# Kernel tuning notes

Measured on AMD Instinct MI355X. Metric: run time of the kernel, lower is better.

Reference implementation:

```python
import jax, jax.numpy as jnp
import numpy as np

N_QUBITS = 10
N_LAYERS = 3
DIM = 2 ** N_QUBITS
B = 2048
T1, T2, GATE_TIME = 0.05, 0.07, 1e-07
P_GATE_1Q, P_GATE_2Q, P_READOUT = 0.001, 0.01, 0.02
P_AMP = 1.0 - np.exp(-GATE_TIME / T1)
P_PHASE = 1.0 - np.exp(-GATE_TIME / T2)

_I = np.eye(2, dtype=np.complex64)
_X = np.array([[0, 1], [1, 0]], np.complex64)
_Y = np.array([[0, -1j], [1j, 0]], np.complex64)
_Z = np.array([[1, 0], [0, -1]], np.complex64)

def _depol(p):
    return [np.sqrt(1 - p) * _I, np.sqrt(p / 3) * _X, np.sqrt(p / 3) * _Y, np.sqrt(p / 3) * _Z]

def _ampdamp(g):
    return [np.array([[1, 0], [0, np.sqrt(1 - g)]], np.complex64), np.array([[0, np.sqrt(g)], [0, 0]], np.complex64)]

def _phasedamp(g):
    return [np.array([[1, 0], [0, np.sqrt(1 - g)]], np.complex64), np.array([[0, 0], [0, np.sqrt(g)]], np.complex64)]

def _bitflip(p):
    return [np.sqrt(1 - p) * _I, np.sqrt(p) * _X]

DEPOL1 = [jnp.asarray(k) for k in _depol(P_GATE_1Q)]
DEPOL2 = [jnp.asarray(k) for k in _depol(P_GATE_2Q)]
AMP = [jnp.asarray(k) for k in _ampdamp(P_AMP)]
PHASE = [jnp.asarray(k) for k in _phasedamp(P_PHASE)]
BITFLIP = [jnp.asarray(k) for k in _bitflip(P_READOUT)]
CNOT = jnp.asarray(np.array([[1, 0, 0, 0], [0, 1, 0, 0], [0, 0, 0, 1], [0, 0, 1, 0]], np.complex64).reshape(2, 2, 2, 2))

def pauli_strings(n):
    out = []
    for q in range(n):
        for ch in 'XZ':
            out.append('I' * q + ch + 'I' * (n - q - 1))
    return out

def pauli_tensor(strings):
    mats = {'I': np.eye(2), 'X': np.array([[0., 1.], [1., 0.]]), 'Z': np.array([[1., 0.], [0., -1.]])}
    Ps = []
    for s in strings:
        P = np.array([[1.0]])
        for ch in s:
            P = np.kron(P, mats[ch])
        Ps.append(P)
    return np.stack(Ps).astype(np.float32)

def _apply1(rho, K, q, n):
    # rho' = K rho K^dagger on wire q; rho has shape (2,)*2n (ket axes 0..n-1, bra axes n..2n-1)
    rho = jnp.moveaxis(jnp.tensordot(K, rho, axes=[[1], [q]]), 0, q)
    rho = jnp.moveaxis(jnp.tensordot(jnp.conj(K), rho, axes=[[1], [n + q]]), 0, n + q)
    return rho

def _apply2(rho, U, q1, q2, n):
    rho = jnp.moveaxis(jnp.tensordot(U, rho, axes=[[2, 3], [q1, q2]]), [0, 1], [q1, q2])
    rho = jnp.moveaxis(jnp.tensordot(jnp.conj(U), rho, axes=[[2, 3], [n + q1, n + q2]]), [0, 1], [n + q1, n + q2])
    return rho

def _chan1(rho, Ks, q, n):
    out = _apply1(rho, Ks[0], q, n)
    for K in Ks[1:]:
        out = out + _apply1(rho, K, q, n)
    return out

def _rot(phi, theta, omega):
    # qml.Rot = RZ(omega) @ RY(theta) @ RZ(phi)
    c = jnp.cos(theta / 2).astype(jnp.complex64)
    s = jnp.sin(theta / 2).astype(jnp.complex64)
    ep = jnp.exp(-0.5j * (phi + omega))
    em = jnp.exp(0.5j * (phi - omega))
    return jnp.stack([jnp.stack([ep * c, -em * s]), jnp.stack([jnp.conj(em) * s, jnp.conj(ep) * c])])

def _simulate(weights):
    nl, nq, _ = weights.shape
    rho = jnp.zeros((2,) * (2 * nq), jnp.complex64).at[(0,) * (2 * nq)].set(1.0)
    for l in range(nl):
        for q in range(nq):
            rho = _apply1(rho, _rot(weights[l, q, 0], weights[l, q, 1], weights[l, q, 2]), q, nq)
            rho = _chan1(rho, DEPOL1, q, nq)
            rho = _chan1(rho, AMP, q, nq)
            rho = _chan1(rho, PHASE, q, nq)
        for q in range(nq):
            t = (q + 1) % nq
            rho = _apply2(rho, CNOT, q, t, nq)
            for wq in (q, t):
                rho = _chan1(rho, DEPOL2, wq, nq)
            for wq in (q, t):
                rho = _chan1(rho, AMP, wq, nq)
            for wq in (q, t):
                rho = _chan1(rho, PHASE, wq, nq)
    for q in range(nq):
        rho = _chan1(rho, BITFLIP, q, nq)
    return rho.reshape(2 ** nq, 2 ** nq)

def setup_inputs() -> dict:
    key = jax.random.key(0)
    k1, k2, k3 = jax.random.split(key, 3)
    x = jax.random.normal(k1, (B, DIM), jnp.float32)
    circuit_weights = jax.random.uniform(k2, (N_LAYERS, N_QUBITS, 3), jnp.float32)
    w = jax.random.normal(k3, (2 * N_QUBITS,), jnp.float32) * 0.01
    b = jnp.zeros((DIM,), jnp.float32)
    P_tensor = jnp.asarray(pauli_tensor(pauli_strings(N_QUBITS)))  # [K, dim, dim]
    return {"x": x, "b": b, "w": w, "circuit_weights": circuit_weights, "P_tensor": P_tensor}

def reference(x, b, w, circuit_weights, P_tensor):
    x_t = x + b  # [B, dim]
    feats = jnp.einsum('bm,kmn,bn->bk', x_t, P_tensor, x_t)  # [B, K]
    rho = _simulate(circuit_weights)  # [dim, dim] complex
    exps = jnp.real(jnp.einsum('kmn,nm->k', P_tensor.astype(jnp.complex64), rho))  # tr(P_k rho)
    logits = jnp.sum(feats * (w * exps), axis=1)
    return jax.nn.sigmoid(logits)
```

## Files before the change

### kernel.cpp

```cpp
#include <hip/hip_runtime.h>
#include <hip/hip_bf16.h>
#include <math.h>

struct cf { float x, y; };
__device__ __forceinline__ cf cfmul(cf a, cf b){ return {a.x*b.x - a.y*b.y, a.x*b.y + a.y*b.x}; }
__device__ __forceinline__ cf cfconj(cf a){ return {a.x, -a.y}; }
__device__ __forceinline__ cf cfadd(cf a, cf b){ return {a.x+b.x, a.y+b.y}; }

__device__ __forceinline__ void pmat(int k, cf* P){
    if (k==0){ P[0]={1.f,0.f}; P[1]={0.f,0.f}; P[2]={0.f,0.f}; P[3]={1.f,0.f}; }
    else if (k==1){ P[0]={0.f,0.f}; P[1]={1.f,0.f}; P[2]={1.f,0.f}; P[3]={0.f,0.f}; }
    else if (k==2){ P[0]={0.f,0.f}; P[1]={0.f,-1.f}; P[2]={0.f,1.f}; P[3]={0.f,0.f}; }
    else { P[0]={1.f,0.f}; P[1]={0.f,0.f}; P[2]={0.f,0.f}; P[3]={-1.f,0.f}; }
}
__device__ void mul2(cf* C, const cf* A, const cf* B){
    C[0]=cfadd(cfmul(A[0],B[0]),cfmul(A[1],B[2]));
    C[1]=cfadd(cfmul(A[0],B[1]),cfmul(A[1],B[3]));
    C[2]=cfadd(cfmul(A[2],B[0]),cfmul(A[3],B[2]));
    C[3]=cfadd(cfmul(A[2],B[1]),cfmul(A[3],B[3]));
}
__device__ void ptm_acc(float* T, const cf* K){
    cf Kd[4] = {cfconj(K[0]), cfconj(K[2]), cfconj(K[1]), cfconj(K[3])};
    for (int s=0;s<4;s++){
        cf Ps[4]; pmat(s,Ps);
        cf t1[4], t2[4];
        mul2(t1, K, Ps);
        mul2(t2, t1, Kd);
        for (int t=0;t<4;t++){
            cf Pt[4]; pmat(t,Pt);
            float re = Pt[0].x*t2[0].x - Pt[0].y*t2[0].y
                     + Pt[1].x*t2[2].x - Pt[1].y*t2[2].y
                     + Pt[2].x*t2[1].x - Pt[2].y*t2[1].y
                     + Pt[3].x*t2[3].x - Pt[3].y*t2[3].y;
            T[t*4+s] += 0.5f*re;
        }
    }
}
__device__ void rmm4(float* C, const float* A, const float* B){
    for (int i=0;i<4;i++) for (int j=0;j<4;j++){
        float s=0.f;
        for (int k=0;k<4;k++) s += A[i*4+k]*B[k*4+j];
        C[i*4+j]=s;
    }
}

__device__ void prep_compute(float* sm, const float* __restrict__ wts, int tid){
    if (tid < 31){
        const float GA = -expm1f(-2.0000000000000002e-06f);
        const float GP = -expm1f(-1.4285714285714286e-06f);
        float sa = sqrtf(1.f-GA), spp = sqrtf(1.f-GP);
        float p = (tid==30) ? 0.01f : 0.001f;
        float f = 1.f - (4.f/3.f)*p;
        float Tn[16] = {0};
        Tn[0]      = 1.f;
        Tn[1*4+1]  = spp*sa*f;
        Tn[2*4+2]  = spp*sa*f;
        Tn[3*4+3]  = (1.f-GA)*f;
        Tn[3*4+0]  = GA;
        if (tid == 30){
            for (int i=0;i<16;i++) sm[480+i] = Tn[i];
        } else {
            float phi = wts[tid*3+0], th = wts[tid*3+1], om = wts[tid*3+2];
            float ct = cosf(0.5f*th), st = sinf(0.5f*th);
            cf ep = {cosf(0.5f*(phi+om)), -sinf(0.5f*(phi+om))};
            cf em = {cosf(0.5f*(phi-om)),  sinf(0.5f*(phi-om))};
            cf U[4];
            U[0] = { ep.x*ct,  ep.y*ct};
            U[1] = {-em.x*st, -em.y*st};
            U[2] = { em.x*st, -em.y*st};
            U[3] = { ep.x*ct, -ep.y*ct};
            float Tr[16] = {0};
            ptm_acc(Tr, U);
            float S[16]; rmm4(S, Tn, Tr);
            for (int i=0;i<16;i++) sm[tid*16+i] = S[i];
        }
    }
}

__device__ __forceinline__ unsigned swz(unsigned t){ return t ^ ((t>>7)&0x1Cu); }

#define ALONG_A(Mp) { _Pragma("unroll") for (int db_=0; db_<4; db_++){ \
    float a0=v[db_], a1=v[4+db_], a2=v[8+db_], a3=v[12+db_]; \
    _Pragma("unroll") for (int dp_=0; dp_<4; dp_++){ \
        v[dp_*4+db_] = (Mp)[dp_*4+0]*a0 + (Mp)[dp_*4+1]*a1 + (Mp)[dp_*4+2]*a2 + (Mp)[dp_*4+3]*a3; } } }

#define ALONG_B(Mp) { _Pragma("unroll") for (int da_=0; da_<4; da_++){ \
    float a0=v[da_*4+0], a1=v[da_*4+1], a2=v[da_*4+2], a3=v[da_*4+3]; \
    _Pragma("unroll") for (int dp_=0; dp_<4; dp_++){ \
        v[da_*4+dp_] = (Mp)[dp_*4+0]*a0 + (Mp)[dp_*4+1]*a1 + (Mp)[dp_*4+2]*a2 + (Mp)[dp_*4+3]*a3; } } }

#define ALONG_AT(Mp) { _Pragma("unroll") for (int db_=0; db_<4; db_++){ \
    float a0=v[db_], a1=v[4+db_], a2=v[8+db_], a3=v[12+db_]; \
    _Pragma("unroll") for (int dp_=0; dp_<4; dp_++){ \
        v[dp_*4+db_] = (Mp)[0*4+dp_]*a0 + (Mp)[1*4+dp_]*a1 + (Mp)[2*4+dp_]*a2 + (Mp)[3*4+dp_]*a3; } } }

#define ALONG_BT(Mp) { _Pragma("unroll") for (int da_=0; da_<4; da_++){ \
    float a0=v[da_*4+0], a1=v[da_*4+1], a2=v[da_*4+2], a3=v[da_*4+3]; \
    _Pragma("unroll") for (int dp_=0; dp_<4; dp_++){ \
        v[da_*4+dp_] = (Mp)[0*4+dp_]*a0 + (Mp)[1*4+dp_]*a1 + (Mp)[2*4+dp_]*a2 + (Mp)[3*4+dp_]*a3; } } }

#define CNOT_PERM { float t0; \
    t0=v[4];  v[4]=v[5];   v[5]=t0;  \
    t0=v[8];  v[8]=v[9];   v[9]=t0;  \
    t0=v[2];  v[2]=v[14];  v[14]=t0; \
    t0=v[3];  v[3]=v[15];  v[15]=t0; \
    t0=v[6];  v[6]=v[11];  v[11]=t0; \
    t0=v[7];  v[7]=-v[10]; v[10]=-t0; }

template<int LAYER, int ISB>
__device__ __forceinline__ void run_ops(float* tile, const float* sm, int tid){
    constexpr int A_PA[5] = {0,10,8,6,4}, A_PB[5] = {10,8,6,4,2};
    constexpr int B_PA[5] = {2,10,8,6,4}, B_PB[5] = {10,8,6,4,0};
#pragma unroll
    for (int i=0; i<5; i++){
        const int pa = ISB ? B_PA[i] : A_PA[i];
        const int pb = ISB ? B_PB[i] : A_PB[i];
        const int mA = (!ISB && i==0) ? LAYER*160 : -1;
        const int mB = !ISB ? (LAYER*10 + i + 1)*16
                            : ((i < 4) ? (LAYER*10 + 6 + i)*16 : -1);
        const int lo = pa < pb ? pa : pb, hi = pa < pb ? pb : pa;
        unsigned g8 = (unsigned)tid;
        unsigned xx = ((g8 >> lo) << (lo+2)) | (g8 & ((1u<<lo)-1u));
        xx = ((xx >> hi) << (hi+2)) | (xx & ((1u<<hi)-1u));
        unsigned adr[16];
        float v[16];
#pragma unroll
        for (int d=0; d<16; d++){
            unsigned t = xx | ((unsigned)(d>>2) << pa) | ((unsigned)(d&3) << pb);
            adr[d] = swz(t);
            v[d] = tile[adr[d]];
        }
        if (mA >= 0){ const float* M = sm + mA; ALONG_A(M); }
        if (mB >= 0){ const float* M = sm + mB; ALONG_B(M); }
        CNOT_PERM
        { const float* M = sm + 480; ALONG_B(M); ALONG_A(M); }
#pragma unroll
        for (int d=0; d<16; d++) tile[adr[d]] = v[d];
        __syncthreads();
    }
}

template<int LAYER, int ISB, int DOINIT, int MODE>
__global__ void __launch_bounds__(256)
fused6(float* __restrict__ rho, const float* __restrict__ wts,
       float* __restrict__ smg, float* __restrict__ cvec,
       float* __restrict__ Vbuf, float* __restrict__ part)
{
    __shared__ __align__(16) float tile[4096];
    __shared__ __align__(16) float sm[496];
    __shared__ float redp[192];
    int tid = threadIdx.x;
    unsigned blk = blockIdx.x;

    if (DOINIT){
        prep_compute(sm, wts, tid);
    } else {
        if (tid < 124)
            reinterpret_cast<float4*>(sm)[tid] = reinterpret_cast<const float4*>(smg)[tid];
    }

    if constexpr (DOINIT != 0){
        if (blk >= 256){
            int k = (int)blk - 256;
            unsigned sk = ((k & 1) ? 3u : 1u) << (2*(k>>1));
#pragma unroll
            for (int r=0; r<16; r++){
                unsigned u = tid + 256u*r;
                tile[swz(u)] = (u == sk) ? 1.f : 0.f;
            }
            __syncthreads();
            const int B_PA[5] = {2,10,8,6,4}, B_PB[5] = {10,8,6,4,0};
            for (int i=4; i>=0; i--){
                int pa = B_PA[i], pb = B_PB[i];
                int mB = (i < 4) ? (26 + i)*16 : -1;
                int lo = pa < pb ? pa : pb, hi = pa < pb ? pb : pa;
                unsigned g8 = (unsigned)tid;
                unsigned xx = ((g8 >> lo) << (lo+2)) | (g8 & ((1u<<lo)-1u));
                xx = ((xx >> hi) << (hi+2)) | (xx & ((1u<<hi)-1u));
                unsigned adr[16];
                float v[16];
                for (int d=0; d<16; d++){
                    unsigned t = xx | ((unsigned)(d>>2) << pa) | ((unsigned)(d&3) << pb);
                    adr[d] = swz(t);
                    v[d] = tile[adr[d]];
                }
                { const float* M = sm + 480; ALONG_AT(M); ALONG_BT(M); }
                CNOT_PERM
                if (mB >= 0){ const float* M = sm + mB; ALONG_BT(M); }
                for (int d=0; d<16; d++) tile[adr[d]] = v[d];
                __syncthreads();
            }
#pragma unroll
            for (int r=0; r<4; r++){
                unsigned u = 4u*(tid + 256u*r);
                *reinterpret_cast<float4*>(Vbuf + k*4096 + u) =
                    *reinterpret_cast<const float4*>(&tile[swz(u)]);
            }
            return;
        }
    }

    unsigned bo = blk << (ISB ? 4 : 12);
    if (DOINIT){
#pragma unroll
        for (int r=0; r<16; r++){
            unsigned u = tid + 256u*r;
            unsigned g = u | bo;
            unsigned e = g & 0x55555u, o = (g>>1) & 0x55555u;
            tile[swz(u)] = (e==o) ? 1.f : 0.f;
        }
    } else {
#pragma unroll
        for (int r=0; r<4; r++){
            unsigned u = 4u*(tid + 256u*r);
            unsigned g = ISB ? ((u & 15u) | ((u>>4)<<12) | bo) : (u | bo);
            *reinterpret_cast<float4*>(&tile[swz(u)]) = *reinterpret_cast<const float4*>(rho + g);
        }
    }
    __syncthreads();

    if (DOINIT && blk == 0 && tid < 124)
        reinterpret_cast<float4*>(smg)[tid] = *reinterpret_cast<const float4*>(&sm[4*tid]);

    run_ops<LAYER, ISB>(tile, sm, tid);

    if (MODE == 3){
        if (blk == 0 && tid < 8){
            const unsigned TI[8] = {1024u,3072u,256u,768u,64u,192u,16u,48u};
            cvec[2 + tid] = tile[swz(TI[tid])];
        }
        if (tid < 192){
            int k = tid >> 4, j = tid & 15;
            redp[tid] = Vbuf[k*4096 + (int)blk*16 + j] * tile[j];
        }
        __syncthreads();
        if (tid < 12){
            float s = 0.f;
#pragma unroll
            for (int j=0; j<16; j++) s += redp[tid*16 + j];
            part[tid*256 + (int)blk] = s;
        }
        return;
    }

#pragma unroll
    for (int r=0; r<4; r++){
        unsigned u = 4u*(tid + 256u*r);
        unsigned g = ISB ? ((u & 15u) | ((u>>4)<<12) | bo) : (u | bo);
        *reinterpret_cast<float4*>(rho + g) = *reinterpret_cast<const float4*>(&tile[swz(u)]);
    }
}

__global__ void __launch_bounds__(256)
logits_mega(const float* __restrict__ part, const float* __restrict__ cvec,
            const float* __restrict__ x, const float* __restrict__ bvec,
            const float* __restrict__ w, float* __restrict__ out)
{
    __shared__ float xs[1024];
    __shared__ float cvw[20];
    __shared__ float redl[80];
    __shared__ float redp[192];
    int tid = threadIdx.x;
    int b = (int)blockIdx.x;

    if (tid < 192){
        int k = tid >> 4, j = tid & 15;
        float s = 0.f;
#pragma unroll
        for (int m=0; m<16; m++) s += part[k*256 + j*16 + m];
        redp[tid] = s;
    }
    {
        float4 xv = reinterpret_cast<const float4*>(x + (size_t)b*1024)[tid];
        float4 bv = reinterpret_cast<const float4*>(bvec)[tid];
        xs[tid*4+0] = xv.x + bv.x;
        xs[tid*4+1] = xv.y + bv.y;
        xs[tid*4+2] = xv.z + bv.z;
        xs[tid*4+3] = xv.w + bv.w;
    }
    __syncthreads();
    if (tid < 12){
        float s = 0.f;
#pragma unroll
        for (int j=0; j<16; j++) s += redp[tid*16 + j];
        const int TQ[6] = {0,5,9,8,7,6};
        int ci = 2*TQ[tid>>1] + (tid & 1);
        cvw[ci] = ((tid & 1) ? 0.96f : 1.0f) * w[ci] * s;
    } else if (tid < 20){
        int ci = tid - 10;
        cvw[ci] = ((ci & 1) ? 0.96f : 1.0f) * w[ci] * cvec[ci];
    }

    float aX[10] = {0,0,0,0,0,0,0,0,0,0};
    float aZ[10] = {0,0,0,0,0,0,0,0,0,0};
#pragma unroll
    for (int r=0; r<4; r++){
        int m = tid + r*256;
        float xm = xs[m];
        float x2 = xm*xm;
#pragma unroll
        for (int q=0; q<10; q++){
            int bit = 1 << (9-q);
            aX[q] += xm * xs[m ^ bit];
            aZ[q] += (m & bit) ? -x2 : x2;
        }
    }
    int lane = tid & 63, wv = tid >> 6;
#pragma unroll
    for (int kk=0; kk<20; kk++){
        float v = (kk < 10) ? aX[kk] : aZ[kk-10];
        v += __shfl_down(v, 32); v += __shfl_down(v, 16); v += __shfl_down(v, 8);
        v += __shfl_down(v, 4);  v += __shfl_down(v, 2);  v += __shfl_down(v, 1);
        if (lane == 0) redl[wv*20 + kk] = v;
    }
    __syncthreads();
    if (tid == 0){
        float logit = 0.f;
#pragma unroll
        for (int q=0; q<10; q++){
            float FX = redl[q]    + redl[20+q] + redl[40+q] + redl[60+q];
            float FZ = redl[10+q] + redl[30+q] + redl[50+q] + redl[70+q];
            logit += cvw[2*q] * FX + cvw[2*q+1] * FZ;
        }
        out[b] = 1.f / (1.f + expf(-logit));
    }
}

extern "C" void kernel_launch(void* const* d_in, const int* in_sizes, int n_in,
                              void* d_out, int out_size, void* d_ws, size_t ws_size,
                              hipStream_t stream) {
    const float* x    = (const float*)d_in[0];
    const float* bvec = (const float*)d_in[1];
    const float* w    = (const float*)d_in[2];
    const float* cw   = (const float*)d_in[3];
    float* out = (float*)d_out;

    char* ws = (char*)d_ws;
    float* rho  = (float*)ws;
    float* smg  = (float*)(ws + (size_t)(1u<<20)*sizeof(float));
    float* cvec = smg + 512;
    float* part = cvec + 32;
    float* Vbuf = part + 3072;
    (void)ws_size; (void)in_sizes; (void)n_in; (void)out_size;

    fused6<0,0,1,0><<<268, 256, 0, stream>>>(rho, cw, smg, cvec, Vbuf, part);
    fused6<0,1,0,0><<<256, 256, 0, stream>>>(rho, cw, smg, cvec, Vbuf, part);
    fused6<1,0,0,0><<<256, 256, 0, stream>>>(rho, cw, smg, cvec, Vbuf, part);
    fused6<1,1,0,0><<<256, 256, 0, stream>>>(rho, cw, smg, cvec, Vbuf, part);
    fused6<2,0,0,3><<<256, 256, 0, stream>>>(rho, cw, smg, cvec, Vbuf, part);
    logits_mega<<<2048, 256, 0, stream>>>(part, cvec, x, bvec, w, out);
}
```

Baseline: 70.25 us.

## Co-schedule Vbuf back-propagation with layer-0 state blocks in a dual 512-thread kernel

The first launch used to run 268 blocks: 256 density-matrix tiles plus 12 extra blocks that back-propagate the Pauli observables into Vbuf. A new phase0_dual kernel runs 256 blocks of 512 threads instead. The lower half of each block handles the state tile, and the upper half of blocks 0-11 handles the Vbuf tile in a separate shared buffer. This is meant to remove the trailing second wave of 12 blocks beyond the CU count. The cost is more shared memory and registers per block. The permutation tables also move from constexpr locals to __constant__ arrays, which may or may not stay compile-time folded.

New measurement: 67.96 us. 3.3% less time.

```diff
diff --git a/kernel.cpp b/kernel.cpp
--- a/kernel.cpp
+++ b/kernel.cpp
@@ -107,14 +107,15 @@
     t0=v[6];  v[6]=v[11];  v[11]=t0; \
     t0=v[7];  v[7]=-v[10]; v[10]=-t0; }
 
+__device__ __constant__ const int cA_PA[5] = {0,10,8,6,4}, cA_PB[5] = {10,8,6,4,2};
+__device__ __constant__ const int cB_PA[5] = {2,10,8,6,4}, cB_PB[5] = {10,8,6,4,0};
+
 template<int LAYER, int ISB>
 __device__ __forceinline__ void run_ops(float* tile, const float* sm, int tid){
-    constexpr int A_PA[5] = {0,10,8,6,4}, A_PB[5] = {10,8,6,4,2};
-    constexpr int B_PA[5] = {2,10,8,6,4}, B_PB[5] = {10,8,6,4,0};
 #pragma unroll
     for (int i=0; i<5; i++){
-        const int pa = ISB ? B_PA[i] : A_PA[i];
-        const int pb = ISB ? B_PB[i] : A_PB[i];
+        const int pa = ISB ? cB_PA[i] : cA_PA[i];
+        const int pb = ISB ? cB_PB[i] : cA_PB[i];
         const int mA = (!ISB && i==0) ? LAYER*160 : -1;
         const int mB = !ISB ? (LAYER*10 + i + 1)*16
                             : ((i < 4) ? (LAYER*10 + 6 + i)*16 : -1);
@@ -140,11 +141,115 @@
     }
 }
 
-template<int LAYER, int ISB, int DOINIT, int MODE>
+__global__ void __launch_bounds__(512, 1)
+phase0_dual(float* __restrict__ rho, const float* __restrict__ wts,
+            float* __restrict__ smg, float* __restrict__ Vbuf)
+{
+    __shared__ __align__(16) float tileS[4096];
+    __shared__ __align__(16) float tileV[4096];
+    __shared__ __align__(16) float sm[496];
+    int tid = threadIdx.x;
+    unsigned blk = blockIdx.x;
+    const bool lower = (tid < 256);
+    const int lt = tid & 255;
+
+    prep_compute(sm, wts, tid);
+
+    if (lower){
+        unsigned bo = blk << 12;
+#pragma unroll
+        for (int r=0; r<16; r++){
+            unsigned u = lt + 256u*r;
+            unsigned g = u | bo;
+            unsigned e = g & 0x55555u, o = (g>>1) & 0x55555u;
+            tileS[swz(u)] = (e==o) ? 1.f : 0.f;
+        }
+    } else if (blk < 12){
+        int k = (int)blk;
+        unsigned sk = ((k & 1) ? 3u : 1u) << (2*(k>>1));
+#pragma unroll
+        for (int r=0; r<16; r++){
+            unsigned u = lt + 256u*r;
+            tileV[swz(u)] = (u == sk) ? 1.f : 0.f;
+        }
+    }
+    __syncthreads();
+
+    if (blk == 0 && lower && lt < 124)
+        reinterpret_cast<float4*>(smg)[lt] = *reinterpret_cast<const float4*>(&sm[4*lt]);
+
+#pragma unroll
+    for (int it=0; it<5; ++it){
+        if (lower){
+            const int i = it;
+            const int pa = cA_PA[i], pb = cA_PB[i];
+            const int mA = (i==0) ? 0 : -1;
+            const int mB = (i + 1)*16;
+            const int lo = pa < pb ? pa : pb, hi = pa < pb ? pb : pa;
+            unsigned g8 = (unsigned)lt;
+            unsigned xx = ((g8 >> lo) << (lo+2)) | (g8 & ((1u<<lo)-1u));
+            xx = ((xx >> hi) << (hi+2)) | (xx & ((1u<<hi)-1u));
+            unsigned adr[16];
+            float v[16];
+#pragma unroll
+            for (int d=0; d<16; d++){
+                unsigned t = xx | ((unsigned)(d>>2) << pa) | ((unsigned)(d&3) << pb);
+                adr[d] = swz(t);
+                v[d] = tileS[adr[d]];
+            }
+            if (mA >= 0){ const float* M = sm + mA; ALONG_A(M); }
+            { const float* M = sm + mB; ALONG_B(M); }
+            CNOT_PERM
+            { const float* M = sm + 480; ALONG_B(M); ALONG_A(M); }
+#pragma unroll
+            for (int d=0; d<16; d++) tileS[adr[d]] = v[d];
+        } else if (blk < 12){
+            const int i = 4 - it;
+            const int pa = cB_PA[i], pb = cB_PB[i];
+            const int mB = (i < 4) ? (26 + i)*16 : -1;
+            const int lo = pa < pb ? pa : pb, hi = pa < pb ? pb : pa;
+            unsigned g8 = (unsigned)lt;
+            unsigned xx = ((g8 >> lo) << (lo+2)) | (g8 & ((1u<<lo)-1u));
+            xx = ((xx >> hi) << (hi+2)) | (xx & ((1u<<hi)-1u));
+            unsigned adr[16];
+            float v[16];
+#pragma unroll
+            for (int d=0; d<16; d++){
+                unsigned t = xx | ((unsigned)(d>>2) << pa) | ((unsigned)(d&3) << pb);
+                adr[d] = swz(t);
+                v[d] = tileV[adr[d]];
+            }
+            { const float* M = sm + 480; ALONG_AT(M); ALONG_BT(M); }
+            CNOT_PERM
+            if (mB >= 0){ const float* M = sm + mB; ALONG_BT(M); }
+#pragma unroll
+            for (int d=0; d<16; d++) tileV[adr[d]] = v[d];
+        }
+        __syncthreads();
+    }
+
+    if (lower){
+        unsigned bo = blk << 12;
+#pragma unroll
+        for (int r=0; r<4; r++){
+            unsigned u = 4u*(lt + 256u*r);
+            *reinterpret_cast<float4*>(rho + (u | bo)) =
+                *reinterpret_cast<const float4*>(&tileS[swz(u)]);
+        }
+    } else if (blk < 12){
+#pragma unroll
+        for (int r=0; r<4; r++){
+            unsigned u = 4u*(lt + 256u*r);
+            *reinterpret_cast<float4*>(Vbuf + (int)blk*4096 + u) =
+                *reinterpret_cast<const float4*>(&tileV[swz(u)]);
+        }
+    }
+}
+
+template<int LAYER, int ISB, int MODE>
 __global__ void __launch_bounds__(256)
-fused6(float* __restrict__ rho, const float* __restrict__ wts,
-       float* __restrict__ smg, float* __restrict__ cvec,
-       float* __restrict__ Vbuf, float* __restrict__ part)
+fused6(float* __restrict__ rho, const float* __restrict__ smg, float* __restrict__ cvec,
+       const float* __restrict__ Vbuf, float* __restrict__ part)
 {
     __shared__ __align__(16) float tile[4096];
     __shared__ __align__(16) float sm[496];
@@ -152,75 +257,17 @@
     int tid = threadIdx.x;
     unsigned blk = blockIdx.x;
 
-    if (DOINIT){
-        prep_compute(sm, wts, tid);
-    } else {
-        if (tid < 124)
-            reinterpret_cast<float4*>(sm)[tid] = reinterpret_cast<const float4*>(smg)[tid];
-    }
-
-    if constexpr (DOINIT != 0){
-        if (blk >= 256){
-            int k = (int)blk - 256;
-            unsigned sk = ((k & 1) ? 3u : 1u) << (2*(k>>1));
-#pragma unroll
-            for (int r=0; r<16; r++){
-                unsigned u = tid + 256u*r;
-                tile[swz(u)] = (u == sk) ? 1.f : 0.f;
-            }
-            __syncthreads();
-            const int B_PA[5] = {2,10,8,6,4}, B_PB[5] = {10,8,6,4,0};
-            for (int i=4; i>=0; i--){
-                int pa = B_PA[i], pb = B_PB[i];
-                int mB = (i < 4) ? (26 + i)*16 : -1;
-                int lo = pa < pb ? pa : pb, hi = pa < pb ? pb : pa;
-                unsigned g8 = (unsigned)tid;
-                unsigned xx = ((g8 >> lo) << (lo+2)) | (g8 & ((1u<<lo)-1u));
-                xx = ((xx >> hi) << (hi+2)) | (xx & ((1u<<hi)-1u));
-                unsigned adr[16];
-                float v[16];
-                for (int d=0; d<16; d++){
-                    unsigned t = xx | ((unsigned)(d>>2) << pa) | ((unsigned)(d&3) << pb);
-                    adr[d] = swz(t);
-                    v[d] = tile[adr[d]];
-                }
-                { const float* M = sm + 480; ALONG_AT(M); ALONG_BT(M); }
-                CNOT_PERM
-                if (mB >= 0){ const float* M = sm + mB; ALONG_BT(M); }
-                for (int d=0; d<16; d++) tile[adr[d]] = v[d];
-                __syncthreads();
-            }
-#pragma unroll
-            for (int r=0; r<4; r++){
-                unsigned u = 4u*(tid + 256u*r);
-                *reinterpret_cast<float4*>(Vbuf + k*4096 + u) =
-                    *reinterpret_cast<const float4*>(&tile[swz(u)]);
-            }
-            return;
-        }
-    }
+    if (tid < 124)
+        reinterpret_cast<float4*>(sm)[tid] = reinterpret_cast<const float4*>(smg)[tid];
 
     unsigned bo = blk << (ISB ? 4 : 12);
-    if (DOINIT){
-#pragma unroll
-        for (int r=0; r<16; r++){
-            unsigned u = tid + 256u*r;
-            unsigned g = u | bo;
-            unsigned e = g & 0x55555u, o = (g>>1) & 0x55555u;
-            tile[swz(u)] = (e==o) ? 1.f : 0.f;
-        }
-    } else {
-#pragma unroll
-        for (int r=0; r<4; r++){
-            unsigned u = 4u*(tid + 256u*r);
-            unsigned g = ISB ? ((u & 15u) | ((u>>4)<<12) | bo) : (u | bo);
-            *reinterpret_cast<float4*>(&tile[swz(u)]) = *reinterpret_cast<const float4*>(rho + g);
-        }
+#pragma unroll
+    for (int r=0; r<4; r++){
+        unsigned u = 4u*(tid + 256u*r);
+        unsigned g = ISB ? ((u & 15u) | ((u>>4)<<12) | bo) : (u | bo);
+        *reinterpret_cast<float4*>(&tile[swz(u)]) = *reinterpret_cast<const float4*>(rho + g);
     }
     __syncthreads();
-
-    if (DOINIT && blk == 0 && tid < 124)
-        reinterpret_cast<float4*>(smg)[tid] = *reinterpret_cast<const float4*>(&sm[4*tid]);
 
     run_ops<LAYER, ISB>(tile, sm, tid);
 
@@ -343,10 +390,10 @@
     float* Vbuf = part + 3072;
     (void)ws_size; (void)in_sizes; (void)n_in; (void)out_size;
 
-    fused6<0,0,1,0><<<268, 256, 0, stream>>>(rho, cw, smg, cvec, Vbuf, part);
-    fused6<0,1,0,0><<<256, 256, 0, stream>>>(rho, cw, smg, cvec, Vbuf, part);
-    fused6<1,0,0,0><<<256, 256, 0, stream>>>(rho, cw, smg, cvec, Vbuf, part);
-    fused6<1,1,0,0><<<256, 256, 0, stream>>>(rho, cw, smg, cvec, Vbuf, part);
-    fused6<2,0,0,3><<<256, 256, 0, stream>>>(rho, cw, smg, cvec, Vbuf, part);
+    phase0_dual<<<256, 512, 0, stream>>>(rho, cw, smg, Vbuf);
+    fused6<0,1,0><<<256, 256, 0, stream>>>(rho, smg, cvec, Vbuf, part);
+    fused6<1,0,0><<<256, 256, 0, stream>>>(rho, smg, cvec, Vbuf, part);
+    fused6<1,1,0><<<256, 256, 0, stream>>>(rho, smg, cvec, Vbuf, part);
+    fused6<2,0,3><<<256, 256, 0, stream>>>(rho, smg, cvec, Vbuf, part);
     logits_mega<<<2048, 256, 0, stream>>>(part, cvec, x, bvec, w, out);
 }
```
